# Performance work log

Hardware: AMD Instinct MI355X
Metric: run time of the kernel (lower is better)

Reference implementation:

```python
import jax, jax.numpy as jnp
import numpy as np

HID = 384
KV = 384
HEADS = 2
LAYERS = 2
KFFN = 9
WIN = 0.2
SIGMA = 0.3
EPS = 1e-5
HDIM = HID // HEADS


def _sin_pos(T, dim):
    # fairseq SinusoidalPositionalEmbedding; inputs are nonzero floats so all
    # positions are "non-pad": positions = arange(T) + padding_idx + 1 = 1..T
    pos = jnp.arange(1, T + 1, dtype=jnp.float32)
    half = dim // 2
    freqs = jnp.exp(-np.log(10000.0) / (half - 1) * jnp.arange(half, dtype=jnp.float32))
    ang = pos[:, None] * freqs[None, :]
    return jnp.concatenate([jnp.sin(ang), jnp.cos(ang)], axis=-1)  # [T, dim]


def _ln(x, g, b):
    m = jnp.mean(x, axis=-1, keepdims=True)
    v = jnp.var(x, axis=-1, keepdims=True)
    return (x - m) * jax.lax.rsqrt(v + EPS) * g + b


def _window_mask(T1, T2):
    # per-query sliding window over keys (vectorized form of the Python loop)
    w = int(T2 * WIN) // 2
    t = jnp.arange(T1)
    c = (t * T2) // T1                      # win_center = int(t/T1*T2)
    lo = jnp.maximum(0, c - w)
    j = jnp.arange(T2)
    allowed = (j[None, :] >= lo[:, None]) & (j[None, :] < (c + w)[:, None])
    return ~allowed                          # True = masked out, [T1, T2]


def _forward(x1, x2, pos_alpha, ln1_g, ln1_b, qw, kw, vw, ow,
             ln2_g, ln2_b, cw, cb, lw, lb, lnf_g, lnf_b):
    B, T1, C = x1.shape
    T2 = x2.shape[1]
    # no padding (random-normal inputs never have zero abs-sum rows), so all
    # nonpadding multiplies are identity and key_padding_mask is a no-op.
    x1 = x1 + pos_alpha * _sin_pos(T1, C)[None]
    x2 = x2 + pos_alpha * _sin_pos(T2, KV)[None]

    mask = _window_mask(T1, T2)              # [T1, T2] bool
    scaling = HDIM ** -0.5
    guided_loss = jnp.float32(0.0)
    # guided attention mask (lengths == full lengths, no padding)
    ti = jnp.arange(T1, dtype=jnp.float32)[:, None] / T1
    sj = jnp.arange(T2, dtype=jnp.float32)[None, :] / T2
    gmask = 1.0 - jnp.exp(-((sj - ti) ** 2) / (2.0 * SIGMA ** 2))  # [T1, T2]

    aw = None
    for i in range(LAYERS):
        residual = x1
        qn = _ln(x1, ln1_g[i], ln1_b[i])
        q = jnp.einsum('btc,dc->btd', qn, qw[i]) * scaling
        k = jnp.einsum('bsc,dc->bsd', x2, kw[i])
        v = jnp.einsum('bsc,dc->bsd', x2, vw[i])
        q = q.reshape(B, T1, HEADS, HDIM)
        k = k.reshape(B, T2, HEADS, HDIM)
        v = v.reshape(B, T2, HEADS, HDIM)
        scores = jnp.einsum('bqhd,bkhd->bhqk', q, k)
        scores = jnp.where(mask[None, None], jnp.float32(-1e9), scores)
        p = jax.nn.softmax(scores, axis=-1)                  # [B,H,T1,T2]
        attn = jnp.einsum('bhqk,bkhd->bqhd', p, v).reshape(B, T1, C)
        attn = jnp.einsum('btc,dc->btd', attn, ow[i])
        x1 = residual + attn
        if i == 0:  # num_guided_layers = 1
            aw = p.mean(axis=1)                              # head-avg [B,T1,T2]
            guided_loss = guided_loss + (aw * gmask[None]).mean()
        # FFN: Conv1d(C->4C, k=9, SAME) * k^-0.5 -> gelu -> Linear(4C->C)
        residual = x1
        y = _ln(x1, ln2_g[i], ln2_b[i])
        yt = jnp.transpose(y, (0, 2, 1))                     # [B,C,T1]
        h = jax.lax.conv_general_dilated(yt, cw[i], (1,), 'SAME',
                                         dimension_numbers=('NCH', 'OIH', 'NCH'))
        h = (h + cb[i][None, :, None]) * (KFFN ** -0.5)
        h = jax.nn.gelu(jnp.transpose(h, (0, 2, 1)), approximate=False)  # [B,T1,4C]
        y = jnp.einsum('btf,cf->btc', h, lw[i]) + lb[i]
        x1 = residual + y

    x1 = _ln(x1, lnf_g, lnf_b)
    return x1, guided_loss


def setup_inputs() -> dict:
    key = jax.random.key(0)
    ks = jax.random.split(key, 16)
    s = 0.02
    B, T1, T2 = 8, 2048, 512
    return {
        'x1': jax.random.normal(ks[0], (B, T1, HID), jnp.float32),
        'x2': jax.random.normal(ks[1], (B, T2, KV), jnp.float32),
        'pos_alpha': jnp.float32(1.0),
        'ln1_g': jnp.ones((LAYERS, HID), jnp.float32),
        'ln1_b': jnp.zeros((LAYERS, HID), jnp.float32),
        'qw': jax.random.normal(ks[2], (LAYERS, HID, HID), jnp.float32) * s,
        'kw': jax.random.normal(ks[3], (LAYERS, HID, KV), jnp.float32) * s,
        'vw': jax.random.normal(ks[4], (LAYERS, HID, KV), jnp.float32) * s,
        'ow': jax.random.normal(ks[5], (LAYERS, HID, HID), jnp.float32) * s,
        'ln2_g': jnp.ones((LAYERS, HID), jnp.float32),
        'ln2_b': jnp.zeros((LAYERS, HID), jnp.float32),
        'cw': jax.random.normal(ks[6], (LAYERS, 4 * HID, HID, KFFN), jnp.float32) * s,
        'cb': jnp.zeros((LAYERS, 4 * HID), jnp.float32),
        'lw': jax.random.normal(ks[7], (LAYERS, HID, 4 * HID), jnp.float32) * s,
        'lb': jnp.zeros((LAYERS, HID), jnp.float32),
        'lnf_g': jnp.ones((HID,), jnp.float32),
        'lnf_b': jnp.zeros((HID,), jnp.float32),
    }


def reference(x1, x2, pos_alpha, ln1_g, ln1_b, qw, kw, vw, ow,
              ln2_g, ln2_b, cw, cb, lw, lb, lnf_g, lnf_b):
    return _forward(x1, x2, pos_alpha, ln1_g, ln1_b, qw, kw, vw, ow,
                    ln2_g, ln2_b, cw, cb, lw, lb, lnf_g, lnf_b)
```

## Files before the change

kernel.cpp:

```cpp
#include <hip/hip_runtime.h>
#include <math.h>

#define NB 8
#define NT1 2048
#define NT2 512
#define NC 384
#define ND 192
#define NF 1536
#define NKI 3456
#define TPAD 2056

typedef __attribute__((ext_vector_type(8))) short bf16x8;
typedef __attribute__((ext_vector_type(4))) float f32x4;

#define GLOAD16(gsrc, ldst) \
  __builtin_amdgcn_global_load_lds((const __attribute__((address_space(1))) void*)(gsrc), \
                                   (__attribute__((address_space(3))) void*)(ldst), 16, 0, 0)

static __device__ __forceinline__ unsigned short f2bf(float f) {
  unsigned int u = __float_as_uint(f);
  unsigned int r = (u + 0x7fffu + ((u >> 16) & 1u)) >> 16;
  return (unsigned short)r;
}

static __device__ __forceinline__ float warp_sum(float v) {
#pragma unroll
  for (int off = 32; off > 0; off >>= 1) v += __shfl_xor(v, off);
  return v;
}

__global__ __launch_bounds__(256) void k_add_pos2(const float* __restrict__ x,
    const float* __restrict__ alpha_p, float* __restrict__ y, int T, int total2) {
  int i = blockIdx.x * 256 + threadIdx.x;
  if (i >= total2) return;
  int j = i % 192;
  int row = i / 192;
  int t = row % T;
  float freq = __expf(-0.0482216773f * (float)j);
  float ang = (float)(t + 1) * freq;
  float sn, cs;
  __sincosf(ang, &sn, &cs);
  float a = alpha_p[0];
  size_t base = (size_t)row * NC;
  y[base + j] = x[base + j] + a * sn;
  y[base + j + 192] = x[base + j + 192] + a * cs;
}

__global__ __launch_bounds__(256) void k_add_pos2_bf16(const float* __restrict__ x,
    const float* __restrict__ alpha_p, unsigned short* __restrict__ y, int T, int total2) {
  int i = blockIdx.x * 256 + threadIdx.x;
  if (i >= total2) return;
  int j = i % 192;
  int row = i / 192;
  int t = row % T;
  float freq = __expf(-0.0482216773f * (float)j);
  float ang = (float)(t + 1) * freq;
  float sn, cs;
  __sincosf(ang, &sn, &cs);
  float a = alpha_p[0];
  size_t base = (size_t)row * NC;
  y[base + j] = f2bf(x[base + j] + a * sn);
  y[base + j + 192] = f2bf(x[base + j + 192] + a * cs);
}

__global__ __launch_bounds__(256) void k_ln(const float* __restrict__ x,
    const float* __restrict__ g, const float* __restrict__ b,
    float* __restrict__ y, int nrows) {
  int row = blockIdx.x * 4 + (threadIdx.x >> 6);
  int lane = threadIdx.x & 63;
  if (row >= nrows) return;
  const float* xr = x + (size_t)row * NC;
  float v[6];
  float s = 0.f, s2 = 0.f;
#pragma unroll
  for (int i = 0; i < 6; ++i) {
    float t = xr[lane + 64 * i];
    v[i] = t; s += t; s2 += t * t;
  }
  s = warp_sum(s); s2 = warp_sum(s2);
  float mean = s * (1.f / NC);
  float var = s2 * (1.f / NC) - mean * mean;
  float rs = rsqrtf(var + 1e-5f);
  float* yr = y + (size_t)row * NC;
#pragma unroll
  for (int i = 0; i < 6; ++i) {
    int cc = lane + 64 * i;
    yr[cc] = (v[i] - mean) * rs * g[cc] + b[cc];
  }
}

__global__ __launch_bounds__(256) void k_ln_bf16(const float* __restrict__ x,
    const float* __restrict__ g, const float* __restrict__ b,
    unsigned short* __restrict__ y) {
  int row = blockIdx.x * 4 + (threadIdx.x >> 6);
  int lane = threadIdx.x & 63;
  const float* xr = x + (size_t)row * NC;
  float v[6];
  float s = 0.f, s2 = 0.f;
#pragma unroll
  for (int i = 0; i < 6; ++i) {
    float t = xr[lane + 64 * i];
    v[i] = t; s += t; s2 += t * t;
  }
  s = warp_sum(s); s2 = warp_sum(s2);
  float mean = s * (1.f / NC);
  float var = s2 * (1.f / NC) - mean * mean;
  float rs = rsqrtf(var + 1e-5f);
  unsigned short* yr = y + (size_t)row * NC;
#pragma unroll
  for (int i = 0; i < 6; ++i) {
    int cc = lane + 64 * i;
    yr[cc] = f2bf((v[i] - mean) * rs * g[cc] + b[cc]);
  }
}

__global__ __launch_bounds__(256) void k_ln_bf16p(const float* __restrict__ x,
    const float* __restrict__ g, const float* __restrict__ b,
    unsigned short* __restrict__ ypad) {
  int row = blockIdx.x * 4 + (threadIdx.x >> 6);
  int lane = threadIdx.x & 63;
  const float* xr = x + (size_t)row * NC;
  float v[6];
  float s = 0.f, s2 = 0.f;
#pragma unroll
  for (int i = 0; i < 6; ++i) {
    float t = xr[lane + 64 * i];
    v[i] = t; s += t; s2 += t * t;
  }
  s = warp_sum(s); s2 = warp_sum(s2);
  float mean = s * (1.f / NC);
  float var = s2 * (1.f / NC) - mean * mean;
  float rs = rsqrtf(var + 1e-5f);
  int bb = row >> 11, t = row & 2047;
  unsigned short* yr = ypad + ((size_t)(bb * TPAD + t + 4)) * NC;
#pragma unroll
  for (int i = 0; i < 6; ++i) {
    int cc = lane + 64 * i;
    yr[cc] = f2bf((v[i] - mean) * rs * g[cc] + b[cc]);
  }
}

__global__ __launch_bounds__(256) void k_zero_guard(unsigned short* __restrict__ ypad) {
  int i = blockIdx.x * 256 + threadIdx.x;
  if (i >= 24576) return;
  int c = i % NC;
  int r = (i / NC) % 8;
  int b = i / (NC * 8);
  int t = (r < 4) ? r : (2048 + r);
  ypad[((size_t)b * TPAD + t) * NC + c] = 0;
}

__global__ __launch_bounds__(256) void k_pack_cw2(const float* __restrict__ cw,
    unsigned short* __restrict__ cwp) {
  __shared__ float s[NKI];
  int f = blockIdx.x;
  const float* src = cw + (size_t)f * NKI;
  for (int i = threadIdx.x; i < NKI; i += 256) s[i] = src[i];
  __syncthreads();
  unsigned short* dst = cwp + (size_t)f * NKI;
  for (int i = threadIdx.x; i < NKI; i += 256) {
    int kk = i / NC, cc = i - kk * NC;
    dst[i] = f2bf(s[cc * 9 + kk]);
  }
}

__global__ __launch_bounds__(256) void k_cvt_qkvo(const float* __restrict__ qw,
    const float* __restrict__ kw, const float* __restrict__ vw,
    const float* __restrict__ ow, unsigned short* __restrict__ dst, float qscale) {
  int i = blockIdx.x * 256 + threadIdx.x;
  if (i >= 4 * 294912) return;
  int w = i / 294912;
  int j = i - w * 294912;
  const float* s = (w == 0) ? qw : (w == 1) ? kw : (w == 2) ? vw : ow;
  float sc = (w == 0) ? qscale : 1.f;
  dst[i] = f2bf(s[j] * sc);
}

__global__ __launch_bounds__(256) void k_cvt(const float* __restrict__ x,
    unsigned short* __restrict__ y, int n) {
  int i = blockIdx.x * 256 + threadIdx.x;
  if (i < n) y[i] = f2bf(x[i]);
}

__global__ __launch_bounds__(256) void k_pgemm_mfma(
    const unsigned short* __restrict__ A,
    const unsigned short* __restrict__ W,
    unsigned short* __restrict__ Cb,
    float* __restrict__ Cf,
    int K, int mode) {
  __shared__ unsigned short As[128 * 32];
  __shared__ unsigned short Bs[128 * 32];
  const int bn = blockIdx.x * 128;
  const int bm = blockIdx.y * 128;
  const int tid = threadIdx.x;
  const int lane = tid & 63, wv = tid >> 6;
  const int wr = (wv >> 1) * 64, wc = (wv & 1) * 64;
  f32x4 acc[4][4] = {};

  const int chunk = wv * 2;
  const int rloc = chunk * 16 + (lane >> 2);
  const int slot = (lane & 3) * 8;
  const size_t abase = ((size_t)(bm + rloc)) * K + slot;
  const size_t bbase = ((size_t)(bn + rloc)) * K + slot;
  unsigned short* AsW0 = &As[chunk * 512];
  unsigned short* AsW1 = &As[(chunk + 1) * 512];
  unsigned short* BsW0 = &Bs[chunk * 512];
  unsigned short* BsW1 = &Bs[(chunk + 1) * 512];

  const int rsel = lane & 15, ksel = (lane >> 4) * 8;

  for (int kt = 0; kt < K; kt += 32) {
    GLOAD16(A + abase + kt, AsW0);
    GLOAD16(A + abase + kt + (size_t)16 * K, AsW1);
    GLOAD16(W + bbase + kt, BsW0);
    GLOAD16(W + bbase + kt + (size_t)16 * K, BsW1);
    __syncthreads();
    bf16x8 af[4], bfr[4];
#pragma unroll
    for (int m = 0; m < 4; ++m)
      af[m] = *(const bf16x8*)&As[(wr + m * 16 + rsel) * 32 + ksel];
#pragma unroll
    for (int n = 0; n < 4; ++n)
      bfr[n] = *(const bf16x8*)&Bs[(wc + n * 16 + rsel) * 32 + ksel];
#pragma unroll
    for (int m = 0; m < 4; ++m)
#pragma unroll
      for (int n = 0; n < 4; ++n)
        acc[m][n] = __builtin_amdgcn_mfma_f32_16x16x32_bf16(af[m], bfr[n], acc[m][n], 0, 0, 0);
    __syncthreads();
  }

  const int col0 = bn + wc + (lane & 15);
  const int row0 = bm + wr + (lane >> 4) * 4;
#pragma unroll
  for (int m = 0; m < 4; ++m) {
#pragma unroll
    for (int n = 0; n < 4; ++n) {
      int col = col0 + n * 16;
#pragma unroll
      for (int r = 0; r < 4; ++r) {
        int row = row0 + m * 16 + r;
        if (mode == 0) {
          Cb[(size_t)row * NC + col] = f2bf(acc[m][n][r]);
        } else {
          size_t oi = (size_t)row * NC + col;
          Cf[oi] = acc[m][n][r] + Cf[oi];
        }
      }
    }
  }
}

__global__ __launch_bounds__(256) void k_pgemm_kv(
    const unsigned short* __restrict__ A,
    const unsigned short* __restrict__ Wk,
    const unsigned short* __restrict__ Wv,
    unsigned short* __restrict__ Kb,
    unsigned short* __restrict__ Vtb) {
  __shared__ unsigned short As[128 * 32];
  __shared__ unsigned short Bs[128 * 32];
  const int z = blockIdx.z;
  const unsigned short* W = z ? Wv : Wk;
  const int bn = blockIdx.x * 128;
  const int bm = blockIdx.y * 128;
  const int tid = threadIdx.x;
  const int lane = tid & 63, wv = tid >> 6;
  const int wr = (wv >> 1) * 64, wc = (wv & 1) * 64;
  f32x4 acc[4][4] = {};

  const int chunk = wv * 2;
  const int rloc = chunk * 16 + (lane >> 2);
  const int slot = (lane & 3) * 8;
  const size_t abase = ((size_t)(bm + rloc)) * NC + slot;
  const size_t bbase = ((size_t)(bn + rloc)) * NC + slot;
  unsigned short* AsW0 = &As[chunk * 512];
  unsigned short* AsW1 = &As[(chunk + 1) * 512];
  unsigned short* BsW0 = &Bs[chunk * 512];
  unsigned short* BsW1 = &Bs[(chunk + 1) * 512];

  const int rsel = lane & 15, ksel = (lane >> 4) * 8;

  for (int kt = 0; kt < NC; kt += 32) {
    GLOAD16(A + abase + kt, AsW0);
    GLOAD16(A + abase + kt + (size_t)16 * NC, AsW1);
    GLOAD16(W + bbase + kt, BsW0);
    GLOAD16(W + bbase + kt + (size_t)16 * NC, BsW1);
    __syncthreads();
    bf16x8 af[4], bfr[4];
#pragma unroll
    for (int m = 0; m < 4; ++m)
      af[m] = *(const bf16x8*)&As[(wr + m * 16 + rsel) * 32 + ksel];
#pragma unroll
    for (int n = 0; n < 4; ++n)
      bfr[n] = *(const bf16x8*)&Bs[(wc + n * 16 + rsel) * 32 + ksel];
#pragma unroll
    for (int m = 0; m < 4; ++m)
#pragma unroll
      for (int n = 0; n < 4; ++n)
        acc[m][n] = __builtin_amdgcn_mfma_f32_16x16x32_bf16(af[m], bfr[n], acc[m][n], 0, 0, 0);
    __syncthreads();
  }

  const int col0 = bn + wc + (lane & 15);
  const int row0 = bm + wr + (lane >> 4) * 4;
#pragma unroll
  for (int m = 0; m < 4; ++m) {
#pragma unroll
    for (int n = 0; n < 4; ++n) {
      int col = col0 + n * 16;
#pragma unroll
      for (int r = 0; r < 4; ++r) {
        int row = row0 + m * 16 + r;
        if (z == 0) {
          Kb[(size_t)row * NC + col] = f2bf(acc[m][n][r]);
        } else {
          Vtb[((size_t)((row >> 9) * 384 + col)) * 512 + (row & 511)] = f2bf(acc[m][n][r]);
        }
      }
    }
  }
}

__global__ __launch_bounds__(512) void k_conv_mfma(
    const unsigned short* __restrict__ Ypad,
    const unsigned short* __restrict__ Wp,
    const float* __restrict__ cb,
    unsigned short* __restrict__ H) {
  __shared__ unsigned short As[3][256 * 64];
  __shared__ unsigned short Bs[3][128 * 64];
  const int bm = blockIdx.x * 256;
  const int bn = blockIdx.y * 128;
  const int b = bm >> 11, t0 = bm & 2047;
  const int tid = threadIdx.x;
  const int lane = tid & 63, wv = tid >> 6;
  const int wvM = wv >> 1, wvN = wv & 1;
  const int rsel = lane & 15, ghi = lane >> 4;
  const int l8 = lane >> 3, g8 = lane & 7;
  const int gsrc = (g8 ^ l8) * 8;

  f32x4 acc[4][4] = {};

  const size_t arow0 = (size_t)(b * TPAD + t0 + wv * 32 + l8);
  const size_t brow0 = (size_t)(bn + wv * 16 + l8);

#define CONV_STAGE(T, RB)                                                     \
  {                                                                           \
    const int kt_ = (T) * 64;                                                 \
    const int kk_ = kt_ / NC;                                                 \
    const int c0_ = kt_ - kk_ * NC;                                           \
    const size_t asrc_ = (arow0 + kk_) * NC + c0_ + gsrc;                     \
    GLOAD16(Ypad + asrc_, &As[RB][(wv * 32) * 64]);                           \
    GLOAD16(Ypad + asrc_ + (size_t)8 * NC, &As[RB][(wv * 32 + 8) * 64]);      \
    GLOAD16(Ypad + asrc_ + (size_t)16 * NC, &As[RB][(wv * 32 + 16) * 64]);    \
    GLOAD16(Ypad + asrc_ + (size_t)24 * NC, &As[RB][(wv * 32 + 24) * 64]);    \
    const size_t bsrc_ = brow0 * NKI + kt_ + gsrc;                            \
    GLOAD16(Wp + bsrc_, &Bs[RB][(wv * 16) * 64]);                             \
    GLOAD16(Wp + bsrc_ + (size_t)8 * NKI, &Bs[RB][(wv * 16 + 8) * 64]);       \
  }

  const int arow = wvM * 64;
  const int brow = wvN * 64;

#define CONV_ITER(T, RC, RS)                                                  \
  {                                                                           \
    if ((T) + 2 < 54) {                                                       \
      CONV_STAGE((T) + 2, RS);                                                \
      asm volatile("s_waitcnt vmcnt(12)" ::: "memory");                       \
    } else if ((T) + 1 < 54) {                                                \
      asm volatile("s_waitcnt vmcnt(6)" ::: "memory");                        \
    } else {                                                                  \
      asm volatile("s_waitcnt vmcnt(0)" ::: "memory");                        \
    }                                                                         \
    __builtin_amdgcn_sched_barrier(0);                                        \
    __builtin_amdgcn_s_barrier();           \
    bf16x8 af[4][2], bfr[4][2];                                               \
    _Pragma("unroll")                                                         \
    for (int m = 0; m < 4; ++m) {                                             \
      int r = arow + m * 16 + rsel;                                           \
      _Pragma("unroll")                                                       \
      for (int k = 0; k < 2; ++k)                                             \
        af[m][k] = *(const bf16x8*)&As[RC][r * 64 + (((k * 4 + ghi) ^ (r & 7)) * 8)]; \
    }                                                                         \
    _Pragma("unroll")                                                         \
    for (int n = 0; n < 4; ++n) {                                             \
      int r = brow + n * 16 + rsel;                                           \
      _Pragma("unroll")                                                       \
      for (int k = 0; k < 2; ++k)                                             \
        bfr[n][k] = *(const bf16x8*)&Bs[RC][r * 64 + (((k * 4 + ghi) ^ (r & 7)) * 8)]; \
    }                                                                         \
    _Pragma("unroll")                                                         \
    for (int k = 0; k < 2; ++k)                                               \
      _Pragma("unroll")                                                       \
      for (int m = 0; m < 4; ++m)                                             \
        _Pragma("unroll")                                                     \
        for (int n = 0; n < 4; ++n)                                           \
          acc[m][n] = __builtin_amdgcn_mfma_f32_16x16x32_bf16(af[m][k], bfr[n][k], acc[m][n], 0, 0, 0); \
    asm volatile("s_waitcnt lgkmcnt(0)" ::: "memory");   \
    __builtin_amdgcn_sched_barrier(0);                                        \
    __builtin_amdgcn_s_barrier();               \
  }

  CONV_STAGE(0, 0);
  CONV_STAGE(1, 1);
  asm volatile("s_waitcnt vmcnt(6)" ::: "memory");
  __builtin_amdgcn_sched_barrier(0);
  __builtin_amdgcn_s_barrier();

  for (int t3 = 0; t3 < 54; t3 += 3) {
    CONV_ITER(t3 + 0, 0, 2);
    CONV_ITER(t3 + 1, 1, 0);
    CONV_ITER(t3 + 2, 2, 1);
  }
#undef CONV_ITER
#undef CONV_STAGE

  const int col0 = bn + wvN * 64 + rsel;
  const int row0 = bm + wvM * 64 + ghi * 4;
#pragma unroll
  for (int m = 0; m < 4; ++m) {
#pragma unroll
    for (int n = 0; n < 4; ++n) {
      int col = col0 + n * 16;
      float cbv = cb[col];
#pragma unroll
      for (int r = 0; r < 4; ++r) {
        int row = row0 + m * 16 + r;
        float xv = (acc[m][n][r] + cbv) * 0.33333333333333333f;
        float ge = 0.5f * xv * (1.f + erff(xv * 0.70710678118654752f));
        H[(size_t)row * NF + col] = f2bf(ge);
      }
    }
  }
}

__global__ __launch_bounds__(256) void k_lin_mfma(
    const unsigned short* __restrict__ H,
    const unsigned short* __restrict__ Wb,
    const float* __restrict__ lb,
    float* __restrict__ x1a) {
  __shared__ unsigned short As[128 * 32];
  __shared__ unsigned short Bs[128 * 32];
  const int bn = blockIdx.x * 128;
  const int bm = blockIdx.y * 128;
  const int tid = threadIdx.x;
  const int lane = tid & 63, wv = tid >> 6;
  const int wr = (wv >> 1) * 64, wc = (wv & 1) * 64;
  f32x4 acc[4][4] = {};

  const int chunk = wv * 2;
  const int rloc = chunk * 16 + (lane >> 2);
  const int slot = (lane & 3) * 8;
  const size_t abase = ((size_t)(bm + rloc)) * NF + slot;
  const size_t bbase = ((size_t)(bn + rloc)) * NF + slot;
  unsigned short* AsW0 = &As[chunk * 512];
  unsigned short* AsW1 = &As[(chunk + 1) * 512];
  unsigned short* BsW0 = &Bs[chunk * 512];
  unsigned short* BsW1 = &Bs[(chunk + 1) * 512];

  const int rsel = lane & 15, ksel = (lane >> 4) * 8;

  for (int kt = 0; kt < NF; kt += 32) {
    GLOAD16(H + abase + kt, AsW0);
    GLOAD16(H + abase + kt + (size_t)16 * NF, AsW1);
    GLOAD16(Wb + bbase + kt, BsW0);
    GLOAD16(Wb + bbase + kt + (size_t)16 * NF, BsW1);
    __syncthreads();
    bf16x8 af[4], bfr[4];
#pragma unroll
    for (int m = 0; m < 4; ++m)
      af[m] = *(const bf16x8*)&As[(wr + m * 16 + rsel) * 32 + ksel];
#pragma unroll
    for (int n = 0; n < 4; ++n)
      bfr[n] = *(const bf16x8*)&Bs[(wc + n * 16 + rsel) * 32 + ksel];
#pragma unroll
    for (int m = 0; m < 4; ++m)
#pragma unroll
      for (int n = 0; n < 4; ++n)
        acc[m][n] = __builtin_amdgcn_mfma_f32_16x16x32_bf16(af[m], bfr[n], acc[m][n], 0, 0, 0);
    __syncthreads();
  }

  const int col0 = bn + wc + (lane & 15);
  const int row0 = bm + wr + (lane >> 4) * 4;
#pragma unroll
  for (int m = 0; m < 4; ++m) {
#pragma unroll
    for (int n = 0; n < 4; ++n) {
      int col = col0 + n * 16;
      float lbv = lb[col];
#pragma unroll
      for (int r = 0; r < 4; ++r) {
        int row = row0 + m * 16 + r;
        size_t oi = (size_t)row * NC + col;
        x1a[oi] = acc[m][n][r] + lbv + x1a[oi];
      }
    }
  }
}

__global__ __launch_bounds__(256) void k_attn_mfma(
    const unsigned short* __restrict__ qbb,
    const unsigned short* __restrict__ kbb,
    const unsigned short* __restrict__ vtb,
    unsigned short* __restrict__ o, int guided, float* __restrict__ gl) {
  __shared__ unsigned short lds[32768];
  const int tid = threadIdx.x;
  const int lane = tid & 63, wv = tid >> 6;
  const int rsel = lane & 15, ghi = lane >> 4;
  const int idx = blockIdx.x;
  const int tg = idx & 31;
  const int bh = idx >> 5;
  const int h = bh & 1, b = bh >> 1;
  const int t0 = tg * 64;
  const int c0 = t0 >> 2;
  int klo = c0 - 51; if (klo < 0) klo = 0;
  klo &= ~7;
  if (klo > 384) klo = 384;

  const unsigned short* qrow = qbb + (size_t)(b * NT1 + t0 + wv * 16 + rsel) * NC + h * ND;
  bf16x8 qf[6];
#pragma unroll
  for (int kk = 0; kk < 6; ++kk)
    qf[kk] = *(const bf16x8*)(qrow + kk * 32 + ghi * 8);

  {
    const size_t kbase = (size_t)(b * NT2 + klo) * NC + h * ND;
#pragma unroll
    for (int it = 0; it < 12; ++it) {
      int g = it * 256 + tid;
      int row = g / 24, go = g % 24;
      int gs = go ^ (row & 7);
      GLOAD16(kbb + kbase + (size_t)row * NC + gs * 8, &lds[(it * 256 + wv * 64) * 8]);
    }
  }
  __syncthreads();

  f32x4 accs[8] = {};
#pragma unroll
  for (int kk = 0; kk < 6; ++kk) {
#pragma unroll
    for (int n = 0; n < 8; ++n) {
      int row = n * 16 + rsel;
      bf16x8 bfr = *(const bf16x8*)&lds[row * 192 + (((kk * 4 + ghi) ^ (rsel & 7)) * 8)];
      accs[n] = __builtin_amdgcn_mfma_f32_16x16x32_bf16(qf[kk], bfr, accs[n], 0, 0, 0);
    }
  }

  unsigned short* pl = &lds[24576 + wv * 2048];
  float gacc = 0.f;
  const int t0w = t0 + wv * 16;
#pragma unroll
  for (int r = 0; r < 4; ++r) {
    int t = t0w + ghi * 4 + r;
    int c = t >> 2;
    int loq = c - 51; if (loq < 0) loq = 0;
    int hiq = c + 51; if (hiq > NT2) hiq = NT2;
    float sv[8];
    float mx = -1e30f;
#pragma unroll
    for (int n = 0; n < 8; ++n) {
      int j = klo + n * 16 + rsel;
      float s = (j >= loq && j < hiq) ? accs[n][r] : -1e30f;
      sv[n] = s; mx = fmaxf(mx, s);
    }
#pragma unroll
    for (int off = 1; off < 16; off <<= 1) mx = fmaxf(mx, __shfl_xor(mx, off));
    float e[8]; float se = 0.f;
#pragma unroll
    for (int n = 0; n < 8; ++n) { e[n] = __expf(sv[n] - mx); se += e[n]; }
#pragma unroll
    for (int off = 1; off < 16; off <<= 1) se += __shfl_xor(se, off);
    float inv = 1.f / se;
    int q = ghi * 4 + r;
#pragma unroll
    for (int n = 0; n < 8; ++n) {
      float pv = e[n] * inv;
      int klocal = n * 16 + rsel;
      pl[q * 128 + (((klocal >> 3) ^ (q & 7)) * 8) + (klocal & 7)] = f2bf(pv);
      if (guided) {
        int j = klo + klocal;
        float d = (float)j * (1.f / NT2) - (float)t * (1.f / NT1);
        gacc += pv * (1.f - __expf(-(d * d) * 5.5555555556f));
      }
    }
  }
  if (guided) {
    gacc = warp_sum(gacc);
    if (lane == 0) atomicAdd(gl, gacc * (1.f / 16777216.f));
  }
  __syncthreads();

  {
    const size_t vbase = ((size_t)(b * 2 + h) * ND) * NT2 + klo;
#pragma unroll
    for (int it = 0; it < 12; ++it) {
      int g = it * 256 + tid;
      int row = g >> 4, go = g & 15;
      int gs = go ^ (row & 7);
      GLOAD16(vtb + vbase + (size_t)row * NT2 + gs * 8, &lds[(it * 256 + wv * 64) * 8]);
    }
  }
  __syncthreads();

  f32x4 acco[12] = {};
#pragma unroll
  for (int kt = 0; kt < 4; ++kt) {
    bf16x8 pa = *(const bf16x8*)&pl[rsel * 128 + (((kt * 4 + ghi) ^ (rsel & 7)) * 8)];
#pragma unroll
    for (int n = 0; n < 12; ++n) {
      int row = n * 16 + rsel;
      bf16x8 bfr = *(const bf16x8*)&lds[row * 128 + (((kt * 4 + ghi) ^ (rsel & 7)) * 8)];
      acco[n] = __builtin_amdgcn_mfma_f32_16x16x32_bf16(pa, bfr, acco[n], 0, 0, 0);
    }
  }

  unsigned short* obase = o + (size_t)(b * NT1 + t0w + ghi * 4) * NC + h * ND;
#pragma unroll
  for (int n = 0; n < 12; ++n) {
#pragma unroll
    for (int r = 0; r < 4; ++r) {
      obase[(size_t)r * NC + n * 16 + rsel] = f2bf(acco[n][r]);
    }
  }
}

extern "C" void kernel_launch(void* const* d_in, const int* in_sizes, int n_in,
                              void* d_out, int out_size, void* d_ws, size_t ws_size,
                              hipStream_t stream) {
  (void)in_sizes; (void)n_in; (void)out_size; (void)ws_size;
  const float* x1    = (const float*)d_in[0];
  const float* x2    = (const float*)d_in[1];
  const float* alpha = (const float*)d_in[2];
  const float* ln1_g = (const float*)d_in[3];
  const float* ln1_b = (const float*)d_in[4];
  const float* qw    = (const float*)d_in[5];
  const float* kw    = (const float*)d_in[6];
  const float* vw    = (const float*)d_in[7];
  const float* ow    = (const float*)d_in[8];
  const float* ln2_g = (const float*)d_in[9];
  const float* ln2_b = (const float*)d_in[10];
  const float* cw    = (const float*)d_in[11];
  const float* cb    = (const float*)d_in[12];
  const float* lw    = (const float*)d_in[13];
  const float* lb    = (const float*)d_in[14];
  const float* lnf_g = (const float*)d_in[15];
  const float* lnf_b = (const float*)d_in[16];
  float* out = (float*)d_out;
  float* gl = out + 6291456;

  float* p = (float*)d_ws;
  float* x1a = p; p += 6291456;
  unsigned short* us = (unsigned short*)p;
  unsigned short* x2b  = us; us += 1572864;
  unsigned short* tmpb = us; us += 6291456;
  unsigned short* ypad = us; us += 8 * TPAD * NC;
  unsigned short* cwpb = us; us += 2 * (size_t)NF * NKI;
  unsigned short* lwb  = us; us += 2 * (size_t)NC * NF;
  unsigned short* hb   = us; us += (size_t)16384 * NF;
  unsigned short* qbb  = us; us += 6291456;
  unsigned short* kbb  = us; us += 1572864;
  unsigned short* vtb  = us; us += 1572864;
  unsigned short* qwb  = us; us += 294912;
  unsigned short* kwb  = us; us += 294912;
  unsigned short* vwb  = us; us += 294912;
  unsigned short* owb  = us; us += 294912;

  hipMemsetAsync(gl, 0, sizeof(float), stream);
  k_zero_guard<<<96, 256, 0, stream>>>(ypad);
  k_add_pos2<<<12288, 256, 0, stream>>>(x1, alpha, x1a, NT1, 3145728);
  k_add_pos2_bf16<<<3072, 256, 0, stream>>>(x2, alpha, x2b, NT2, 786432);

  const float scaling = 0.07216878364870323f;
  k_cvt_qkvo<<<4608, 256, 0, stream>>>(qw, kw, vw, ow, qwb, scaling);
  k_cvt<<<4608, 256, 0, stream>>>(lw, lwb, 1179648);
  k_pack_cw2<<<3072, 256, 0, stream>>>(cw, cwpb);

  for (int l = 0; l < 2; ++l) {
    k_ln_bf16<<<4096, 256, 0, stream>>>(x1a, ln1_g + l * 384, ln1_b + l * 384, tmpb);
    k_pgemm_mfma<<<dim3(3, 128), 256, 0, stream>>>(tmpb, qwb + (size_t)l * 147456, qbb, nullptr, 384, 0);
    k_pgemm_kv<<<dim3(3, 32, 2), 256, 0, stream>>>(x2b, kwb + (size_t)l * 147456,
                                                   vwb + (size_t)l * 147456, kbb, vtb);
    k_attn_mfma<<<512, 256, 0, stream>>>(qbb, kbb, vtb, tmpb, l == 0 ? 1 : 0, gl);
    k_pgemm_mfma<<<dim3(3, 128), 256, 0, stream>>>(tmpb, owb + (size_t)l * 147456, nullptr, x1a, 384, 1);
    k_ln_bf16p<<<4096, 256, 0, stream>>>(x1a, ln2_g + l * 384, ln2_b + l * 384, ypad);
    k_conv_mfma<<<dim3(64, 12), 512, 0, stream>>>(ypad, cwpb + (size_t)l * 5308416, cb + l * 1536, hb);
    k_lin_mfma<<<dim3(3, 128), 256, 0, stream>>>(hb, lwb + (size_t)l * 589824, lb + l * 384, x1a);
  }
  k_ln<<<4096, 256, 0, stream>>>(x1a, lnf_g, lnf_b, out, 16384);
}
```

Baseline: 778.3 us.

## Enlarge conv GEMM tile to 256x256 with quadrant-interleaved double-buffered pipeline

The im2col conv GEMM block tile grows from 256x128 to 256x256, which halves the grid along N and raises operand reuse per LDS byte. The K loop moves from a 3-stage ring to a 2-buffer scheme split into A and B halves. Each K step runs as four MFMA quadrants, with global-to-LDS loads for later stages interleaved between them and s_setprio raised around the MFMA bursts. The cost is more accumulator registers per thread (8x4 fragments), more barriers per K step, and fewer blocks in flight, which may hurt occupancy or tail behaviour.

```diff
diff --git a/kernel.cpp b/kernel.cpp
--- a/kernel.cpp
+++ b/kernel.cpp
@@ -326,106 +326,171 @@
     const unsigned short* __restrict__ Wp,
     const float* __restrict__ cb,
     unsigned short* __restrict__ H) {
-  __shared__ unsigned short As[3][256 * 64];
-  __shared__ unsigned short Bs[3][128 * 64];
+  __shared__ unsigned short As[2][2][8192];
+  __shared__ unsigned short Bs[2][2][8192];
   const int bm = blockIdx.x * 256;
-  const int bn = blockIdx.y * 128;
+  const int bn = blockIdx.y * 256;
   const int b = bm >> 11, t0 = bm & 2047;
   const int tid = threadIdx.x;
   const int lane = tid & 63, wv = tid >> 6;
-  const int wvM = wv >> 1, wvN = wv & 1;
+  const int wvM = wv >> 2, wvN = wv & 3;
   const int rsel = lane & 15, ghi = lane >> 4;
   const int l8 = lane >> 3, g8 = lane & 7;
   const int gsrc = (g8 ^ l8) * 8;
-
-  f32x4 acc[4][4] = {};
-
-  const size_t arow0 = (size_t)(b * TPAD + t0 + wv * 32 + l8);
-  const size_t brow0 = (size_t)(bn + wv * 16 + l8);
-
-#define CONV_STAGE(T, RB)                                                     \
+  const int x0 = (ghi ^ (rsel & 7)) * 8;
+  const int x1 = ((4 + ghi) ^ (rsel & 7)) * 8;
+
+  f32x4 acc[8][4] = {};
+
+  const size_t aglob = (size_t)(b * TPAD + t0 + wv * 16 + l8);
+  const size_t bglob = (size_t)(bn + wv * 16 + l8);
+
+#define STAGE_A(T, h, d)                                                      \
   {                                                                           \
     const int kt_ = (T) * 64;                                                 \
     const int kk_ = kt_ / NC;                                                 \
     const int c0_ = kt_ - kk_ * NC;                                           \
-    const size_t asrc_ = (arow0 + kk_) * NC + c0_ + gsrc;                     \
-    GLOAD16(Ypad + asrc_, &As[RB][(wv * 32) * 64]);                           \
-    GLOAD16(Ypad + asrc_ + (size_t)8 * NC, &As[RB][(wv * 32 + 8) * 64]);      \
-    GLOAD16(Ypad + asrc_ + (size_t)16 * NC, &As[RB][(wv * 32 + 16) * 64]);    \
-    GLOAD16(Ypad + asrc_ + (size_t)24 * NC, &As[RB][(wv * 32 + 24) * 64]);    \
-    const size_t bsrc_ = brow0 * NKI + kt_ + gsrc;                            \
-    GLOAD16(Wp + bsrc_, &Bs[RB][(wv * 16) * 64]);                             \
-    GLOAD16(Wp + bsrc_ + (size_t)8 * NKI, &Bs[RB][(wv * 16 + 8) * 64]);       \
-  }
-
-  const int arow = wvM * 64;
-  const int brow = wvN * 64;
-
-#define CONV_ITER(T, RC, RS)                                                  \
+    const size_t s_ = (aglob + (h) * 128 + kk_) * NC + c0_ + gsrc;            \
+    GLOAD16(Ypad + s_, &As[d][h][(wv * 16) * 64]);                            \
+    GLOAD16(Ypad + s_ + (size_t)8 * NC, &As[d][h][(wv * 16 + 8) * 64]);       \
+  }
+#define STAGE_B(T, h, d)                                                      \
   {                                                                           \
-    if ((T) + 2 < 54) {                                                       \
-      CONV_STAGE((T) + 2, RS);                                                \
-      asm volatile("s_waitcnt vmcnt(12)" ::: "memory");                       \
-    } else if ((T) + 1 < 54) {                                                \
-      asm volatile("s_waitcnt vmcnt(6)" ::: "memory");                        \
-    } else {                                                                  \
-      asm volatile("s_waitcnt vmcnt(0)" ::: "memory");                        \
-    }                                                                         \
-    __builtin_amdgcn_sched_barrier(0);                                        \
-    __builtin_amdgcn_s_barrier();           \
-    bf16x8 af[4][2], bfr[4][2];                                               \
-    _Pragma("unroll")                                                         \
-    for (int m = 0; m < 4; ++m) {                                             \
-      int r = arow + m * 16 + rsel;                                           \
-      _Pragma("unroll")                                                       \
-      for (int k = 0; k < 2; ++k)                                             \
-        af[m][k] = *(const bf16x8*)&As[RC][r * 64 + (((k * 4 + ghi) ^ (r & 7)) * 8)]; \
-    }                                                                         \
-    _Pragma("unroll")                                                         \
-    for (int n = 0; n < 4; ++n) {                                             \
-      int r = brow + n * 16 + rsel;                                           \
-      _Pragma("unroll")                                                       \
-      for (int k = 0; k < 2; ++k)                                             \
-        bfr[n][k] = *(const bf16x8*)&Bs[RC][r * 64 + (((k * 4 + ghi) ^ (r & 7)) * 8)]; \
-    }                                                                         \
-    _Pragma("unroll")                                                         \
-    for (int k = 0; k < 2; ++k)                                               \
-      _Pragma("unroll")                                                       \
-      for (int m = 0; m < 4; ++m)                                             \
-        _Pragma("unroll")                                                     \
-        for (int n = 0; n < 4; ++n)                                           \
-          acc[m][n] = __builtin_amdgcn_mfma_f32_16x16x32_bf16(af[m][k], bfr[n][k], acc[m][n], 0, 0, 0); \
-    asm volatile("s_waitcnt lgkmcnt(0)" ::: "memory");   \
-    __builtin_amdgcn_sched_barrier(0);                                        \
-    __builtin_amdgcn_s_barrier();               \
-  }
-
-  CONV_STAGE(0, 0);
-  CONV_STAGE(1, 1);
+    const size_t s_ = (bglob + (h) * 128) * NKI + (T) * 64 + gsrc;            \
+    GLOAD16(Wp + s_, &Bs[d][h][(wv * 16) * 64]);                              \
+    GLOAD16(Wp + s_ + (size_t)8 * NKI, &Bs[d][h][(wv * 16 + 8) * 64]);        \
+  }
+
+  STAGE_A(0, 0, 0); STAGE_B(0, 0, 0); STAGE_B(0, 1, 0); STAGE_A(0, 1, 0);
+  STAGE_A(1, 0, 1); STAGE_B(1, 0, 1); STAGE_B(1, 1, 1);
   asm volatile("s_waitcnt vmcnt(6)" ::: "memory");
   __builtin_amdgcn_sched_barrier(0);
   __builtin_amdgcn_s_barrier();
 
-  for (int t3 = 0; t3 < 54; t3 += 3) {
-    CONV_ITER(t3 + 0, 0, 2);
-    CONV_ITER(t3 + 1, 1, 0);
-    CONV_ITER(t3 + 2, 2, 1);
-  }
-#undef CONV_ITER
-#undef CONV_STAGE
-
-  const int col0 = bn + wvN * 64 + rsel;
-  const int row0 = bm + wvM * 64 + ghi * 4;
-#pragma unroll
-  for (int m = 0; m < 4; ++m) {
-#pragma unroll
-    for (int n = 0; n < 4; ++n) {
-      int col = col0 + n * 16;
+  const int arow_base = wvM * 16 + rsel;
+  const int brow_base = wvN * 16 + rsel;
+
+  for (int T = 0; T < 54; ++T) {
+    const int d = T & 1;
+    const unsigned short* A0p = As[d][0];
+    const unsigned short* A1p = As[d][1];
+    const unsigned short* B0p = Bs[d][0];
+    const unsigned short* B1p = Bs[d][1];
+    bf16x8 a[4][2], b0[2][2], b1[2][2];
+
+#pragma unroll
+    for (int f = 0; f < 4; ++f) {
+      int r = f * 32 + arow_base;
+      a[f][0] = *(const bf16x8*)&A0p[r * 64 + x0];
+      a[f][1] = *(const bf16x8*)&A0p[r * 64 + x1];
+    }
+#pragma unroll
+    for (int g = 0; g < 2; ++g) {
+      int r = g * 64 + brow_base;
+      b0[g][0] = *(const bf16x8*)&B0p[r * 64 + x0];
+      b0[g][1] = *(const bf16x8*)&B0p[r * 64 + x1];
+    }
+    if (T + 1 < 54) STAGE_A(T + 1, 1, (T + 1) & 1);
+    asm volatile("s_waitcnt lgkmcnt(8)" ::: "memory");
+    __builtin_amdgcn_sched_barrier(0);
+    __builtin_amdgcn_s_barrier();
+    asm volatile("s_waitcnt lgkmcnt(0)" ::: "memory");
+    __builtin_amdgcn_sched_barrier(0);
+    __builtin_amdgcn_s_setprio(1);
+#pragma unroll
+    for (int k = 0; k < 2; ++k)
+#pragma unroll
+      for (int f = 0; f < 4; ++f)
+#pragma unroll
+        for (int g = 0; g < 2; ++g)
+          acc[f][g] = __builtin_amdgcn_mfma_f32_16x16x32_bf16(a[f][k], b0[g][k], acc[f][g], 0, 0, 0);
+    __builtin_amdgcn_s_setprio(0);
+    __builtin_amdgcn_sched_barrier(0);
+    __builtin_amdgcn_s_barrier();
+
+#pragma unroll
+    for (int g = 0; g < 2; ++g) {
+      int r = g * 64 + brow_base;
+      b1[g][0] = *(const bf16x8*)&B1p[r * 64 + x0];
+      b1[g][1] = *(const bf16x8*)&B1p[r * 64 + x1];
+    }
+    if (T + 2 < 54) STAGE_A(T + 2, 0, d);
+    __builtin_amdgcn_sched_barrier(0);
+    __builtin_amdgcn_s_barrier();
+    asm volatile("s_waitcnt lgkmcnt(0)" ::: "memory");
+    __builtin_amdgcn_sched_barrier(0);
+    __builtin_amdgcn_s_setprio(1);
+#pragma unroll
+    for (int k = 0; k < 2; ++k)
+#pragma unroll
+      for (int f = 0; f < 4; ++f)
+#pragma unroll
+        for (int g = 0; g < 2; ++g)
+          acc[f][2 + g] = __builtin_amdgcn_mfma_f32_16x16x32_bf16(a[f][k], b1[g][k], acc[f][2 + g], 0, 0, 0);
+    __builtin_amdgcn_s_setprio(0);
+    __builtin_amdgcn_sched_barrier(0);
+    __builtin_amdgcn_s_barrier();
+
+#pragma unroll
+    for (int f = 0; f < 4; ++f) {
+      int r = f * 32 + arow_base;
+      a[f][0] = *(const bf16x8*)&A1p[r * 64 + x0];
+      a[f][1] = *(const bf16x8*)&A1p[r * 64 + x1];
+    }
+    if (T + 2 < 54) STAGE_B(T + 2, 0, d);
+    __builtin_amdgcn_sched_barrier(0);
+    __builtin_amdgcn_s_barrier();
+    asm volatile("s_waitcnt lgkmcnt(0)" ::: "memory");
+    __builtin_amdgcn_sched_barrier(0);
+    __builtin_amdgcn_s_setprio(1);
+#pragma unroll
+    for (int k = 0; k < 2; ++k)
+#pragma unroll
+      for (int f = 0; f < 4; ++f)
+#pragma unroll
+        for (int g = 0; g < 2; ++g)
+          acc[4 + f][g] = __builtin_amdgcn_mfma_f32_16x16x32_bf16(a[f][k], b0[g][k], acc[4 + f][g], 0, 0, 0);
+    __builtin_amdgcn_s_setprio(0);
+    __builtin_amdgcn_sched_barrier(0);
+    __builtin_amdgcn_s_barrier();
+
+    if (T + 2 < 54) STAGE_B(T + 2, 1, d);
+    __builtin_amdgcn_sched_barrier(0);
+    __builtin_amdgcn_s_barrier();
+    __builtin_amdgcn_s_setprio(1);
+#pragma unroll
+    for (int k = 0; k < 2; ++k)
+#pragma unroll
+      for (int f = 0; f < 4; ++f)
+#pragma unroll
+        for (int g = 0; g < 2; ++g)
+          acc[4 + f][2 + g] = __builtin_amdgcn_mfma_f32_16x16x32_bf16(a[f][k], b1[g][k], acc[4 + f][2 + g], 0, 0, 0);
+    __builtin_amdgcn_s_setprio(0);
+    __builtin_amdgcn_sched_barrier(0);
+    if (T + 2 < 54) {
+      asm volatile("s_waitcnt vmcnt(6)" ::: "memory");
+    } else if (T + 1 < 54) {
+      asm volatile("s_waitcnt vmcnt(0)" ::: "memory");
+    }
+    __builtin_amdgcn_sched_barrier(0);
+    __builtin_amdgcn_s_barrier();
+  }
+#undef STAGE_A
+#undef STAGE_B
+
+  const int row00 = bm + wvM * 16 + ghi * 4;
+  const int col00 = bn + wvN * 16 + rsel;
+#pragma unroll
+  for (int mf = 0; mf < 8; ++mf) {
+    int rowb = row00 + (mf >> 2) * 128 + (mf & 3) * 32;
+#pragma unroll
+    for (int g = 0; g < 4; ++g) {
+      int col = col00 + (g >> 1) * 128 + (g & 1) * 64;
       float cbv = cb[col];
 #pragma unroll
       for (int r = 0; r < 4; ++r) {
-        int row = row0 + m * 16 + r;
-        float xv = (acc[m][n][r] + cbv) * 0.33333333333333333f;
+        int row = rowb + r;
+        float xv = (acc[mf][g][r] + cbv) * 0.33333333333333333f;
         float ge = 0.5f * xv * (1.f + erff(xv * 0.70710678118654752f));
         H[(size_t)row * NF + col] = f2bf(ge);
       }
@@ -683,7 +748,7 @@
     k_attn_mfma<<<512, 256, 0, stream>>>(qbb, kbb, vtb, tmpb, l == 0 ? 1 : 0, gl);
     k_pgemm_mfma<<<dim3(3, 128), 256, 0, stream>>>(tmpb, owb + (size_t)l * 147456, nullptr, x1a, 384, 1);
     k_ln_bf16p<<<4096, 256, 0, stream>>>(x1a, ln2_g + l * 384, ln2_b + l * 384, ypad);
-    k_conv_mfma<<<dim3(64, 12), 512, 0, stream>>>(ypad, cwpb + (size_t)l * 5308416, cb + l * 1536, hb);
+    k_conv_mfma<<<dim3(64, 6), 512, 0, stream>>>(ypad, cwpb + (size_t)l * 5308416, cb + l * 1536, hb);
     k_lin_mfma<<<dim3(3, 128), 256, 0, stream>>>(hb, lwb + (size_t)l * 589824, lb + l * 384, x1a);
   }
   k_ln<<<4096, 256, 0, stream>>>(x1a, lnf_g, lnf_b, out, 16384);
```

Result: slower. 794.8 us (+2.1%).
